# Kernel optimization log

Measured on AMD Instinct MI355X. Metric: run time of the kernel, lower is better.

The kernel has to match this reference:

```python
import jax, jax.numpy as jnp
import numpy as np

B, N, M, DN, DE, WN, WE, P = 16, 128, 1024, 512, 256, 128, 128, 512
EMB = WN + WE            # nenn embedding size per node / per edge
CLS_IN = 2 * EMB // 1    # = 2*wn + 2*we = 512
LR_OUT, CR_OUT, MR_OUT = 9, 6, 17
HID = 256


def _mk_params(key):
    ks = jax.random.split(key, 16)
    s = 0.02
    p = {
        'Wn':  jax.random.normal(ks[0], (DN, WN), jnp.float32) * s,
        'We':  jax.random.normal(ks[1], (DE, WE), jnp.float32) * s,
        'Wn2': jax.random.normal(ks[2], (DN, WN), jnp.float32) * s,
        'We2': jax.random.normal(ks[3], (DE, WE), jnp.float32) * s,
    }
    for i, h in enumerate(['scr', 'lr', 'mr']):
        out = {'scr': CR_OUT, 'lr': LR_OUT, 'mr': MR_OUT}[h]
        p[h + '_W1'] = jax.random.normal(ks[4 + 4 * i], (2 * EMB, HID), jnp.float32) * s
        p[h + '_b1'] = jnp.zeros((HID,), jnp.float32)
        p[h + '_W2'] = jax.random.normal(ks[5 + 4 * i], (HID, out), jnp.float32) * s
        p[h + '_b2'] = jnp.zeros((out,), jnp.float32)
    return p


def setup_inputs() -> dict:
    key = jax.random.key(0)
    ks = jax.random.split(key, 10)
    inp = {
        'node_features': jax.random.normal(ks[0], (B, N, DN), jnp.float32),
        'edge_features': jax.random.normal(ks[1], (B, N, N, DE), jnp.float32),
        'adj_mat': (jax.random.uniform(ks[2], (B, N, N)) < 0.1).astype(jnp.float32),
        'line_adj_mat': (jax.random.uniform(ks[3], (B, M, M)) < 0.02).astype(jnp.float32),
        'edge_index': jax.random.randint(ks[4], (B, 2, M), 0, N, jnp.int32),
        'object_pairs': jax.random.randint(ks[5], (B, P, 2), 0, N, jnp.int32),
        'num_obj': jax.random.randint(ks[6], (B,), N // 4, N + 1, jnp.int32),
        'num_edges': jax.random.randint(ks[7], (B,), M // 4, M + 1, jnp.int32),
    }
    inp.update(_mk_params(ks[8]))
    return inp


def _mlp(x, W1, b1, W2, b2):
    return jax.nn.relu(x @ W1 + b1) @ W2 + b2


def _forward(node_features, edge_features, adj_mat, line_adj_mat,
             Wn, We, Wn2, We2,
             scr_W1, scr_b1, scr_W2, scr_b2,
             lr_W1, lr_b1, lr_W2, lr_b2,
             mr_W1, mr_b1, mr_W2, mr_b2,
             edge_index, object_pairs, num_obj, num_edges):
    dt = node_features.dtype
    # ragged slicing [:num_obj] / [:num_edges] expressed as masks (padding stays 0)
    nmask = (jnp.arange(N) < num_obj[:, None]).astype(dt)      # [B,N]
    emask = (jnp.arange(M) < num_edges[:, None]).astype(dt)    # [B,M]

    X = node_features * nmask[..., None]                        # [B,N,DN]
    A = (adj_mat * nmask[:, :, None] * nmask[:, None, :]
         + jnp.eye(N, dtype=dt)[None] * nmask[:, :, None])      # A + I, masked
    h = jax.nn.relu((A @ X) @ Wn) * nmask[..., None]            # [B,N,WN] node-level emb

    src, dst = edge_index[:, 0], edge_index[:, 1]               # [B,M]
    Eg = jax.vmap(lambda e, s, d: e[s, d])(edge_features, src, dst)  # [B,M,DE]
    Eg = Eg * emask[..., None]
    L = (line_adj_mat * emask[:, :, None] * emask[:, None, :]
         + jnp.eye(M, dtype=dt)[None] * emask[:, :, None])      # line graph A + I
    g = jax.nn.relu((L @ Eg) @ We) * emask[..., None]           # [B,M,WE] edge-level emb

    # aggregate edge embeddings onto their source nodes (ragged scatter-add)
    agg = jax.vmap(lambda gb, sb: jnp.zeros((N, WE), gb.dtype).at[sb].add(gb))(g, src)
    node_emb = jnp.concatenate([h, agg * nmask[..., None]], -1)  # [B,N,EMB]

    # dense pairwise edge embeddings [B,N,N,EMB]
    Xp = X @ Wn2                                                 # [B,N,WN]
    Pm = jax.nn.relu(Xp[:, :, None, :] + Xp[:, None, :, :])      # node part [B,N,N,WN]
    Q = jax.nn.relu(edge_features @ We2)                         # edge part [B,N,N,WE]
    edge_emb = jnp.concatenate([Pm, Q], -1)

    # make_classifier_inputs: fused ragged gather instead of python double loop
    p0, p1 = object_pairs[..., 0], object_pairs[..., 1]          # [B,P]
    emb0 = jnp.take_along_axis(node_emb, p0[:, :, None], axis=1)  # [B,P,EMB]
    emb1 = jnp.take_along_axis(node_emb, p1[:, :, None], axis=1)
    eedge = jax.vmap(lambda eb, a, b: eb[a, b])(edge_emb, p0, p1)  # [B,P,EMB]
    ci = jnp.concatenate([emb0 + emb1, eedge], -1)               # aggregator='sum'

    lr = _mlp(ci, lr_W1, lr_b1, lr_W2, lr_b2)
    cr = _mlp(ci, scr_W1, scr_b1, scr_W2, scr_b2)
    mr = _mlp(ci, mr_W1, mr_b1, mr_W2, mr_b2)
    return lr, cr, mr


def reference(node_features, edge_features, adj_mat, line_adj_mat,
              edge_index, object_pairs, num_obj, num_edges,
              Wn, We, Wn2, We2,
              scr_W1, scr_b1, scr_W2, scr_b2,
              lr_W1, lr_b1, lr_W2, lr_b2,
              mr_W1, mr_b1, mr_W2, mr_b2):
    return _forward(node_features, edge_features, adj_mat, line_adj_mat,
                    Wn, We, Wn2, We2,
                    scr_W1, scr_b1, scr_W2, scr_b2,
                    lr_W1, lr_b1, lr_W2, lr_b2,
                    mr_W1, mr_b1, mr_W2, mr_b2,
                    edge_index, object_pairs, num_obj, num_edges)
```

## Files before the change

### kernel.cpp

```cpp
#include <hip/hip_runtime.h>
#include <hip/hip_bf16.h>
#include <cstdint>
#include <cstddef>

#define BB 16
#define NN 128
#define MM 1024
#define DN 512
#define DE 256
#define WN 128
#define WE 128
#define PP 512
#define HIDW 256
#define CIW 512

typedef __attribute__((ext_vector_type(8))) short s16x8;
typedef __attribute__((ext_vector_type(4))) float f32x4;

__device__ __forceinline__ float bf2f(unsigned short u) {
    unsigned int x = ((unsigned int)u) << 16;
    union { unsigned int i; float f; } c; c.i = x; return c.f;
}

__global__ __launch_bounds__(256) void k0_prep(
    const float* __restrict__ lrW1, const float* __restrict__ scrW1,
    const float* __restrict__ mrW1,
    const float* __restrict__ lrb1, const float* __restrict__ scrb1,
    const float* __restrict__ mrb1,
    __hip_bfloat16* __restrict__ W1t, float* __restrict__ b1cat)
{
    int blk = blockIdx.x;
    int t = threadIdx.x;
    if (blk < 768) {
        int h = blk >> 8, n = blk & 255;
        const float* W = (h == 0) ? lrW1 : (h == 1) ? scrW1 : mrW1;
        W1t[(size_t)blk * 512 + t]       = __float2bfloat16(W[t * 256 + n]);
        W1t[(size_t)blk * 512 + t + 256] = __float2bfloat16(W[(t + 256) * 256 + n]);
    } else {
        b1cat[t]       = lrb1[t];
        b1cat[256 + t] = scrb1[t];
        b1cat[512 + t] = mrb1[t];
    }
}

__global__ __launch_bounds__(256) void k1_node_proj(
    const float* __restrict__ nf, const float* __restrict__ Wn,
    const float* __restrict__ Wn2, const int* __restrict__ num_obj,
    float* __restrict__ Y, float* __restrict__ Xp)
{
    __shared__ float Xs[16 * 513];
    int b  = blockIdx.x >> 4;
    int i0 = ((blockIdx.x >> 1) & 7) * 16;
    int ch = blockIdx.x & 1;
    int s  = num_obj[b];
    int t  = threadIdx.x;
    for (int rr = 0; rr < 16; ++rr) {
        int i = i0 + rr;
        const float* row = nf + (size_t)(b * NN + i) * DN;
        Xs[rr * 513 + t]       = (i < s) ? row[t]       : 0.f;
        Xs[rr * 513 + t + 256] = (i < s) ? row[t + 256] : 0.f;
    }
    __syncthreads();
    int c  = ch * 64 + (t & 63);
    int rb = (t >> 6) * 4;
    float a1[4] = {0.f,0.f,0.f,0.f}, a2[4] = {0.f,0.f,0.f,0.f};
    for (int k = 0; k < DN; ++k) {
        float w1 = Wn[k * WN + c];
        float w2 = Wn2[k * WN + c];
        #pragma unroll
        for (int r = 0; r < 4; ++r) {
            float xv = Xs[(rb + r) * 513 + k];
            a1[r] += xv * w1;
            a2[r] += xv * w2;
        }
    }
    #pragma unroll
    for (int r = 0; r < 4; ++r) {
        int i = i0 + rb + r;
        Y [(b * NN + i) * WN + c] = a1[r];
        Xp[(b * NN + i) * WN + c] = a2[r];
    }
}

__global__ __launch_bounds__(256) void k2_gcn_node(
    const float* __restrict__ adj, const int* __restrict__ num_obj,
    const float* __restrict__ Y, float* __restrict__ node_emb)
{
    __shared__ float As[16 * 129];
    int b  = blockIdx.x >> 4;
    int i0 = ((blockIdx.x >> 1) & 7) * 16;
    int ch = blockIdx.x & 1;
    int s  = num_obj[b];
    int t  = threadIdx.x;
    if (t < 128) {
        for (int rr = 0; rr < 16; ++rr) {
            int i = i0 + rr;
            float v = 0.f;
            if (i < s) {
                v = adj[(size_t)(b * NN + i) * NN + t] * ((t < s) ? 1.f : 0.f);
                if (t == i) v += 1.f;
            }
            As[rr * 129 + t] = v;
        }
    }
    __syncthreads();
    int c  = ch * 64 + (t & 63);
    int rb = (t >> 6) * 4;
    float acc[4] = {0.f,0.f,0.f,0.f};
    for (int j = 0; j < NN; ++j) {
        float yv = Y[(b * NN + j) * WN + c];
        #pragma unroll
        for (int r = 0; r < 4; ++r) acc[r] += As[(rb + r) * 129 + j] * yv;
    }
    #pragma unroll
    for (int r = 0; r < 4; ++r) {
        int i = i0 + rb + r;
        node_emb[(b * NN + i) * 256 + c]       = fmaxf(acc[r], 0.f);
        node_emb[(b * NN + i) * 256 + 128 + c] = 0.f;
    }
}

__global__ __launch_bounds__(256) void k3_edge_proj(
    const float* __restrict__ ef, const float* __restrict__ We,
    const int* __restrict__ eidx, const int* __restrict__ num_edges,
    float* __restrict__ G1)
{
    __shared__ float Es[16 * 257];
    int b  = blockIdx.x >> 6;
    int m0 = (blockIdx.x & 63) * 16;
    int se = num_edges[b];
    int t  = threadIdx.x;
    for (int rr = 0; rr < 16; ++rr) {
        int m = m0 + rr;
        float v = 0.f;
        if (m < se) {
            int src = eidx[b * 2 * MM + m];
            int dst = eidx[b * 2 * MM + MM + m];
            v = ef[((size_t)(b * NN + src) * NN + dst) * DE + t];
        }
        Es[rr * 257 + t] = v;
    }
    __syncthreads();
    int c  = t & 127;
    int rb = (t >> 7) * 8;
    float acc[8];
    #pragma unroll
    for (int r = 0; r < 8; ++r) acc[r] = 0.f;
    for (int k = 0; k < DE; ++k) {
        float wv = We[k * WE + c];
        #pragma unroll
        for (int r = 0; r < 8; ++r) acc[r] += Es[(rb + r) * 257 + k] * wv;
    }
    #pragma unroll
    for (int r = 0; r < 8; ++r)
        G1[(size_t)(b * MM + m0 + rb + r) * WE + c] = acc[r];
}

__global__ __launch_bounds__(128) void k4_line_gcn(
    const float* __restrict__ la, const float* __restrict__ G1,
    const int* __restrict__ eidx, const int* __restrict__ num_edges,
    float* __restrict__ node_emb)
{
    int b = blockIdx.x >> 10;
    int m = blockIdx.x & 1023;
    int se = num_edges[b];
    if (m >= se) return;
    __shared__ int   cnt;
    __shared__ int   idxs[MM];
    __shared__ float vals[MM];
    int t = threadIdx.x;
    if (t == 0) cnt = 0;
    __syncthreads();
    const float* larow = la + ((size_t)b * MM + m) * MM;
    for (int it = 0; it < 8; ++it) {
        int j = it * 128 + t;
        float v = larow[j];
        if (v != 0.f) {
            int pos = atomicAdd(&cnt, 1);
            idxs[pos] = j;
            vals[pos] = v;
        }
    }
    __syncthreads();
    int n = cnt;
    const float* g1b = G1 + (size_t)b * MM * WE;
    float acc = g1b[m * WE + t];
    for (int p = 0; p < n; ++p)
        acc += vals[p] * g1b[idxs[p] * WE + t];
    float g = fmaxf(acc, 0.f);
    int src = eidx[b * 2 * MM + m];
    atomicAdd(&node_emb[(b * NN + src) * 256 + 128 + t], g);
}

__global__ __launch_bounds__(256) void k5a_build_ci(
    const float* __restrict__ node_emb, const float* __restrict__ Xp,
    const float* __restrict__ ef, const float* __restrict__ We2,
    const int* __restrict__ opairs, const int* __restrict__ num_obj,
    __hip_bfloat16* __restrict__ ci)
{
    __shared__ float efs[16 * 257];
    __shared__ int   pi0[16], pi1[16];
    __shared__ float nm0[16], nm1[16];
    int b     = blockIdx.x >> 5;
    int pbase = (blockIdx.x & 31) * 16;
    int t     = threadIdx.x;
    int s     = num_obj[b];
    if (t < 16) {
        int p  = pbase + t;
        int i0 = opairs[(b * PP + p) * 2];
        int i1 = opairs[(b * PP + p) * 2 + 1];
        pi0[t] = i0; pi1[t] = i1;
        nm0[t] = (i0 < s) ? 1.f : 0.f;
        nm1[t] = (i1 < s) ? 1.f : 0.f;
    }
    __syncthreads();
    for (int pp = 0; pp < 16; ++pp) {
        int i0 = pi0[pp], i1 = pi1[pp];
        int p  = pbase + pp;
        __hip_bfloat16* cirow = ci + (size_t)(b * PP + p) * CIW;
        efs[pp * 257 + t] = ef[((size_t)(b * NN + i0) * NN + i1) * DE + t];
        float m0f = (t < 128) ? 1.f : nm0[pp];
        float m1f = (t < 128) ? 1.f : nm1[pp];
        float v = node_emb[(b * NN + i0) * 256 + t] * m0f
                + node_emb[(b * NN + i1) * 256 + t] * m1f;
        cirow[t] = __float2bfloat16(v);
        if (t < 128) {
            float pm = Xp[(b * NN + i0) * WN + t] + Xp[(b * NN + i1) * WN + t];
            cirow[256 + t] = __float2bfloat16(fmaxf(pm, 0.f));
        }
    }
    __syncthreads();
    int c   = t & 127;
    int ppb = (t >> 7) * 8;
    float acc[8];
    #pragma unroll
    for (int r = 0; r < 8; ++r) acc[r] = 0.f;
    for (int k = 0; k < DE; ++k) {
        float wv = We2[k * WE + c];
        #pragma unroll
        for (int r = 0; r < 8; ++r) acc[r] += efs[(ppb + r) * 257 + k] * wv;
    }
    #pragma unroll
    for (int r = 0; r < 8; ++r) {
        int p = pbase + ppb + r;
        ci[(size_t)(b * PP + p) * CIW + 384 + c] = __float2bfloat16(fmaxf(acc[r], 0.f));
    }
}

__global__ __launch_bounds__(256) void k6_mlp1_mfma(
    const ushort* __restrict__ A,
    const ushort* __restrict__ Bt,
    const float* __restrict__ b1cat,
    __hip_bfloat16* __restrict__ H)
{
    __shared__ ushort As[128 * 32];
    __shared__ ushort Bs[128 * 32];
    int t    = threadIdx.x;
    int col0 = blockIdx.x * 128;
    int row0 = blockIdx.y * 128;
    int lane = t & 63;
    int w    = t >> 6;
    int wr   = w >> 1, wc = w & 1;
    int arow = w * 32 + (lane >> 2);
    int ak   = (lane & 3) * 8;
    int qk   = (lane >> 4) * 8;
    int fr   = lane & 15;
    f32x4 acc[4][4];
    #pragma unroll
    for (int i = 0; i < 4; ++i)
        #pragma unroll
        for (int j = 0; j < 4; ++j) acc[i][j] = (f32x4){0.f, 0.f, 0.f, 0.f};

    for (int k0 = 0; k0 < CIW; k0 += 32) {
        __syncthreads();
        *(s16x8*)&As[arow * 32 + ak] =
            *(const s16x8*)&A[(size_t)(row0 + arow) * CIW + k0 + ak];
        *(s16x8*)&As[(arow + 16) * 32 + ak] =
            *(const s16x8*)&A[(size_t)(row0 + arow + 16) * CIW + k0 + ak];
        *(s16x8*)&Bs[arow * 32 + ak] =
            *(const s16x8*)&Bt[(size_t)(col0 + arow) * CIW + k0 + ak];
        *(s16x8*)&Bs[(arow + 16) * 32 + ak] =
            *(const s16x8*)&Bt[(size_t)(col0 + arow + 16) * CIW + k0 + ak];
        __syncthreads();
        s16x8 af[4], bfv[4];
        #pragma unroll
        for (int mi = 0; mi < 4; ++mi)
            af[mi] = *(const s16x8*)&As[(wr * 64 + mi * 16 + fr) * 32 + qk];
        #pragma unroll
        for (int ni = 0; ni < 4; ++ni)
            bfv[ni] = *(const s16x8*)&Bs[(wc * 64 + ni * 16 + fr) * 32 + qk];
        #pragma unroll
        for (int mi = 0; mi < 4; ++mi)
            #pragma unroll
            for (int ni = 0; ni < 4; ++ni)
                acc[mi][ni] = __builtin_amdgcn_mfma_f32_16x16x32_bf16(
                    af[mi], bfv[ni], acc[mi][ni], 0, 0, 0);
    }
    int crow = (lane >> 4) * 4;
    #pragma unroll
    for (int mi = 0; mi < 4; ++mi) {
        #pragma unroll
        for (int ni = 0; ni < 4; ++ni) {
            int gc = col0 + wc * 64 + ni * 16 + fr;
            int gr = row0 + wr * 64 + mi * 16 + crow;
            float bias = b1cat[gc];
            #pragma unroll
            for (int rg = 0; rg < 4; ++rg) {
                float v = fmaxf(acc[mi][ni][rg] + bias, 0.f);
                H[(size_t)(gr + rg) * 768 + gc] = __float2bfloat16(v);
            }
        }
    }
}

__global__ __launch_bounds__(256) void k7_mlp2(
    const __hip_bfloat16* __restrict__ H,
    const float* __restrict__ lrW2, const float* __restrict__ lrb2,
    const float* __restrict__ scrW2, const float* __restrict__ scrb2,
    const float* __restrict__ mrW2, const float* __restrict__ mrb2,
    float* __restrict__ outp)
{
    __shared__ float w2s[32 * 257];
    int t = threadIdx.x;
    for (int o = 0; o < 32; ++o) {
        float v;
        if (o < 9)       v = lrW2[t * 9 + o];
        else if (o < 15) v = scrW2[t * 6 + (o - 9)];
        else             v = mrW2[t * 17 + (o - 15)];
        w2s[o * 257 + t] = v;
    }
    __syncthreads();
    int p = blockIdx.x * 8 + (t >> 5);
    int o = t & 31;
    int seg = (o < 9) ? 0 : ((o < 15) ? 1 : 2);
    const ushort* hr = (const ushort*)H + (size_t)p * 768 + seg * 256;
    const float* wr = &w2s[o * 257];
    float acc = (o < 9) ? lrb2[o] : ((o < 15) ? scrb2[o - 9] : mrb2[o - 15]);
    for (int k = 0; k < HIDW; k += 2) {
        ushort2 u = *(const ushort2*)&hr[k];
        acc += bf2f(u.x) * wr[k] + bf2f(u.y) * wr[k + 1];
    }
    if (o < 9)       outp[(size_t)p * 9 + o] = acc;
    else if (o < 15) outp[8192 * 9 + (size_t)p * 6 + (o - 9)] = acc;
    else             outp[8192 * 15 + (size_t)p * 17 + (o - 15)] = acc;
}

extern "C" void kernel_launch(void* const* d_in, const int* in_sizes, int n_in,
                              void* d_out, int out_size, void* d_ws, size_t ws_size,
                              hipStream_t stream) {
    const float* nf    = (const float*)d_in[0];
    const float* ef    = (const float*)d_in[1];
    const float* adj   = (const float*)d_in[2];
    const float* la    = (const float*)d_in[3];
    const int*   eidx  = (const int*)d_in[4];
    const int*   opair = (const int*)d_in[5];
    const int*   nobj  = (const int*)d_in[6];
    const int*   nedg  = (const int*)d_in[7];
    const float* Wn    = (const float*)d_in[8];
    const float* We    = (const float*)d_in[9];
    const float* Wn2   = (const float*)d_in[10];
    const float* We2   = (const float*)d_in[11];
    const float* scrW1 = (const float*)d_in[12];
    const float* scrb1 = (const float*)d_in[13];
    const float* scrW2 = (const float*)d_in[14];
    const float* scrb2 = (const float*)d_in[15];
    const float* lrW1  = (const float*)d_in[16];
    const float* lrb1  = (const float*)d_in[17];
    const float* lrW2  = (const float*)d_in[18];
    const float* lrb2  = (const float*)d_in[19];
    const float* mrW1  = (const float*)d_in[20];
    const float* mrb1  = (const float*)d_in[21];
    const float* mrW2  = (const float*)d_in[22];
    const float* mrb2  = (const float*)d_in[23];

    float* ws = (float*)d_ws;
    float* Y        = ws;
    float* Xp       = Y + 262144;
    float* node_emb = Xp + 262144;
    float* G1       = node_emb + 524288;
    __hip_bfloat16* ci  = (__hip_bfloat16*)(G1 + 2097152);
    __hip_bfloat16* hid = (__hip_bfloat16*)(G1 + 2097152 + 2097152);
    __hip_bfloat16* W1t = (__hip_bfloat16*)(G1 + 2097152 + 2097152 + 3145728);
    float* b1cat    = (float*)(W1t) + 196608;

    k0_prep     <<<769, 256, 0, stream>>>(lrW1, scrW1, mrW1, lrb1, scrb1, mrb1,
                                          W1t, b1cat);
    k1_node_proj<<<BB * 8 * 2, 256, 0, stream>>>(nf, Wn, Wn2, nobj, Y, Xp);
    k2_gcn_node <<<BB * 8 * 2, 256, 0, stream>>>(adj, nobj, Y, node_emb);
    k3_edge_proj<<<BB * (MM / 16), 256, 0, stream>>>(ef, We, eidx, nedg, G1);
    k4_line_gcn <<<BB * MM, 128, 0, stream>>>(la, G1, eidx, nedg, node_emb);
    k5a_build_ci<<<BB * (PP / 16), 256, 0, stream>>>(node_emb, Xp, ef, We2,
                                                     opair, nobj, ci);
    k6_mlp1_mfma<<<dim3(6, 64), 256, 0, stream>>>((const ushort*)ci,
                                                  (const ushort*)W1t, b1cat, hid);
    k7_mlp2     <<<8192 / 8, 256, 0, stream>>>(hid, lrW2, lrb2, scrW2, scrb2,
                                               mrW2, mrb2, (float*)d_out);
}
```

Before: 557.2 us.

## Fuse node, edge and pair projections into one bf16 MFMA gather-GEMM kernel

Replaces the three scalar FP32 projection GEMMs (node features by Wn/Wn2, gathered edge features by We, pair edge features by We2) with a single launch that routes blocks to one of three GEMMs. Each block gathers rows through per-row offsets, applies the validity mask and converts to bf16 before using 16x16x32 bf16 MFMA. The weights are transposed to bf16 in the prep kernel. This removes slow scalar FMA loops and two launches, at the cost of bf16 rounding of the projection inputs and an unpipelined single-buffered K loop.

```diff
diff --git a/kernel.cpp b/kernel.cpp
--- a/kernel.cpp
+++ b/kernel.cpp
@@ -21,13 +21,21 @@
     unsigned int x = ((unsigned int)u) << 16;
     union { unsigned int i; float f; } c; c.i = x; return c.f;
 }
+__device__ __forceinline__ short f2b(float f) {
+    __hip_bfloat16 h = __float2bfloat16(f);
+    return *reinterpret_cast<short*>(&h);
+}
 
 __global__ __launch_bounds__(256) void k0_prep(
     const float* __restrict__ lrW1, const float* __restrict__ scrW1,
     const float* __restrict__ mrW1,
     const float* __restrict__ lrb1, const float* __restrict__ scrb1,
     const float* __restrict__ mrb1,
-    __hip_bfloat16* __restrict__ W1t, float* __restrict__ b1cat)
+    const float* __restrict__ Wn, const float* __restrict__ Wn2,
+    const float* __restrict__ We, const float* __restrict__ We2,
+    __hip_bfloat16* __restrict__ W1t, __hip_bfloat16* __restrict__ WncT,
+    __hip_bfloat16* __restrict__ WeT, __hip_bfloat16* __restrict__ We2T,
+    float* __restrict__ b1cat)
 {
     int blk = blockIdx.x;
     int t = threadIdx.x;
@@ -36,49 +44,143 @@
         const float* W = (h == 0) ? lrW1 : (h == 1) ? scrW1 : mrW1;
         W1t[(size_t)blk * 512 + t]       = __float2bfloat16(W[t * 256 + n]);
         W1t[(size_t)blk * 512 + t + 256] = __float2bfloat16(W[(t + 256) * 256 + n]);
-    } else {
+    } else if (blk == 768) {
         b1cat[t]       = lrb1[t];
         b1cat[256 + t] = scrb1[t];
         b1cat[512 + t] = mrb1[t];
-    }
-}
-
-__global__ __launch_bounds__(256) void k1_node_proj(
-    const float* __restrict__ nf, const float* __restrict__ Wn,
-    const float* __restrict__ Wn2, const int* __restrict__ num_obj,
-    float* __restrict__ Y, float* __restrict__ Xp)
-{
-    __shared__ float Xs[16 * 513];
-    int b  = blockIdx.x >> 4;
-    int i0 = ((blockIdx.x >> 1) & 7) * 16;
-    int ch = blockIdx.x & 1;
-    int s  = num_obj[b];
-    int t  = threadIdx.x;
-    for (int rr = 0; rr < 16; ++rr) {
-        int i = i0 + rr;
-        const float* row = nf + (size_t)(b * NN + i) * DN;
-        Xs[rr * 513 + t]       = (i < s) ? row[t]       : 0.f;
-        Xs[rr * 513 + t + 256] = (i < s) ? row[t + 256] : 0.f;
-    }
-    __syncthreads();
-    int c  = ch * 64 + (t & 63);
-    int rb = (t >> 6) * 4;
-    float a1[4] = {0.f,0.f,0.f,0.f}, a2[4] = {0.f,0.f,0.f,0.f};
-    for (int k = 0; k < DN; ++k) {
-        float w1 = Wn[k * WN + c];
-        float w2 = Wn2[k * WN + c];
-        #pragma unroll
-        for (int r = 0; r < 4; ++r) {
-            float xv = Xs[(rb + r) * 513 + k];
-            a1[r] += xv * w1;
-            a2[r] += xv * w2;
-        }
-    }
+    } else if (blk < 897) {
+        int n = blk - 769;
+        WeT[(size_t)n * 256 + t] = __float2bfloat16(We[t * 128 + n]);
+    } else if (blk < 1153) {
+        int n = blk - 897;
+        const float* W = (n < 128) ? Wn : Wn2;
+        int c = n & 127;
+        WncT[(size_t)n * 512 + t]       = __float2bfloat16(W[t * 128 + c]);
+        WncT[(size_t)n * 512 + t + 256] = __float2bfloat16(W[(t + 256) * 128 + c]);
+    } else {
+        int n = blk - 1153;
+        We2T[(size_t)n * 256 + t] = __float2bfloat16(We2[t * 128 + n]);
+    }
+}
+
+__global__ __launch_bounds__(256) void fproj(
+    const float* __restrict__ nf, const float* __restrict__ ef,
+    const int* __restrict__ eidx, const int* __restrict__ opair,
+    const int* __restrict__ nobj, const int* __restrict__ nedg,
+    const ushort* __restrict__ WncT, const ushort* __restrict__ WeT,
+    const ushort* __restrict__ We2T,
+    float* __restrict__ Y, float* __restrict__ Xp,
+    float* __restrict__ G1, __hip_bfloat16* __restrict__ ci)
+{
+    __shared__ ushort As[128 * 32];
+    __shared__ ushort Bs[128 * 32];
+    __shared__ unsigned rowoff[128];
+    __shared__ float    rowval[128];
+
+    int blk = blockIdx.x;
+    int route, mb, nb, K;
+    const ushort* Bt;
+    if (blk < 32)       { route = 0; mb = blk >> 1;  nb = blk & 1; K = 512; Bt = WncT; }
+    else if (blk < 160) { route = 1; mb = blk - 32;  nb = 0;       K = 256; Bt = WeT;  }
+    else                { route = 2; mb = blk - 160; nb = 0;       K = 256; Bt = We2T; }
+    int row0 = mb * 128, col0 = nb * 128;
+    int t = threadIdx.x;
+
+    if (t < 128) {
+        int r = row0 + t;
+        unsigned off; float valid = 1.f;
+        if (route == 0) {
+            int b = r >> 7, i = r & 127;
+            off = (unsigned)r * DN;
+            valid = (i < nobj[b]) ? 1.f : 0.f;
+        } else if (route == 1) {
+            int b = r >> 10, m = r & 1023;
+            int src = eidx[b * 2 * MM + m];
+            int dst = eidx[b * 2 * MM + MM + m];
+            off = (unsigned)((b * NN + src) * NN + dst) * DE;
+            valid = (m < nedg[b]) ? 1.f : 0.f;
+        } else {
+            int r2 = r;
+            int b = r2 >> 9, p = r2 & 511;
+            int i0 = opair[(b * PP + p) * 2];
+            int i1 = opair[(b * PP + p) * 2 + 1];
+            off = (unsigned)((b * NN + i0) * NN + i1) * DE;
+        }
+        rowoff[t] = off; rowval[t] = valid;
+    }
+
+    const float* Asrc = (route == 0) ? nf : ef;
+    int lane = t & 63;
+    int w    = t >> 6;
+    int wr   = w >> 1, wc = w & 1;
+    int arow = w * 32 + (lane >> 2);
+    int ak   = (lane & 3) * 8;
+    int qk   = (lane >> 4) * 8;
+    int fr   = lane & 15;
+    f32x4 acc[4][4];
     #pragma unroll
-    for (int r = 0; r < 4; ++r) {
-        int i = i0 + rb + r;
-        Y [(b * NN + i) * WN + c] = a1[r];
-        Xp[(b * NN + i) * WN + c] = a2[r];
+    for (int i = 0; i < 4; ++i)
+        #pragma unroll
+        for (int j = 0; j < 4; ++j) acc[i][j] = (f32x4){0.f, 0.f, 0.f, 0.f};
+
+    for (int k0 = 0; k0 < K; k0 += 32) {
+        __syncthreads();
+        {
+            unsigned o0 = rowoff[arow] + k0 + ak;
+            unsigned o1 = rowoff[arow + 16] + k0 + ak;
+            float m0 = rowval[arow], m1 = rowval[arow + 16];
+            float4 a0 = *(const float4*)&Asrc[o0];
+            float4 a1 = *(const float4*)&Asrc[o0 + 4];
+            float4 b0 = *(const float4*)&Asrc[o1];
+            float4 b1 = *(const float4*)&Asrc[o1 + 4];
+            s16x8 pa, pb;
+            pa[0]=f2b(a0.x*m0); pa[1]=f2b(a0.y*m0); pa[2]=f2b(a0.z*m0); pa[3]=f2b(a0.w*m0);
+            pa[4]=f2b(a1.x*m0); pa[5]=f2b(a1.y*m0); pa[6]=f2b(a1.z*m0); pa[7]=f2b(a1.w*m0);
+            pb[0]=f2b(b0.x*m1); pb[1]=f2b(b0.y*m1); pb[2]=f2b(b0.z*m1); pb[3]=f2b(b0.w*m1);
+            pb[4]=f2b(b1.x*m1); pb[5]=f2b(b1.y*m1); pb[6]=f2b(b1.z*m1); pb[7]=f2b(b1.w*m1);
+            *(s16x8*)&As[arow * 32 + ak]        = pa;
+            *(s16x8*)&As[(arow + 16) * 32 + ak] = pb;
+            *(s16x8*)&Bs[arow * 32 + ak] =
+                *(const s16x8*)&Bt[(size_t)(col0 + arow) * K + k0 + ak];
+            *(s16x8*)&Bs[(arow + 16) * 32 + ak] =
+                *(const s16x8*)&Bt[(size_t)(col0 + arow + 16) * K + k0 + ak];
+        }
+        __syncthreads();
+        s16x8 af[4], bfv[4];
+        #pragma unroll
+        for (int mi = 0; mi < 4; ++mi)
+            af[mi] = *(const s16x8*)&As[(wr * 64 + mi * 16 + fr) * 32 + qk];
+        #pragma unroll
+        for (int ni = 0; ni < 4; ++ni)
+            bfv[ni] = *(const s16x8*)&Bs[(wc * 64 + ni * 16 + fr) * 32 + qk];
+        #pragma unroll
+        for (int mi = 0; mi < 4; ++mi)
+            #pragma unroll
+            for (int ni = 0; ni < 4; ++ni)
+                acc[mi][ni] = __builtin_amdgcn_mfma_f32_16x16x32_bf16(
+                    af[mi], bfv[ni], acc[mi][ni], 0, 0, 0);
+    }
+    int crow = (lane >> 4) * 4;
+    #pragma unroll
+    for (int mi = 0; mi < 4; ++mi) {
+        #pragma unroll
+        for (int ni = 0; ni < 4; ++ni) {
+            int gc = col0 + wc * 64 + ni * 16 + fr;
+            int gr = row0 + wr * 64 + mi * 16 + crow;
+            #pragma unroll
+            for (int rg = 0; rg < 4; ++rg) {
+                float v = acc[mi][ni][rg];
+                int r = gr + rg;
+                if (route == 0) {
+                    if (gc < 128) Y [(size_t)r * WN + gc]       = v;
+                    else          Xp[(size_t)r * WN + gc - 128] = v;
+                } else if (route == 1) {
+                    G1[(size_t)r * WE + gc] = v;
+                } else {
+                    ci[(size_t)r * CIW + 384 + gc] = __float2bfloat16(fmaxf(v, 0.f));
+                }
+            }
+        }
     }
 }
 
@@ -118,42 +220,6 @@
         node_emb[(b * NN + i) * 256 + c]       = fmaxf(acc[r], 0.f);
         node_emb[(b * NN + i) * 256 + 128 + c] = 0.f;
     }
-}
-
-__global__ __launch_bounds__(256) void k3_edge_proj(
-    const float* __restrict__ ef, const float* __restrict__ We,
-    const int* __restrict__ eidx, const int* __restrict__ num_edges,
-    float* __restrict__ G1)
-{
-    __shared__ float Es[16 * 257];
-    int b  = blockIdx.x >> 6;
-    int m0 = (blockIdx.x & 63) * 16;
-    int se = num_edges[b];
-    int t  = threadIdx.x;
-    for (int rr = 0; rr < 16; ++rr) {
-        int m = m0 + rr;
-        float v = 0.f;
-        if (m < se) {
-            int src = eidx[b * 2 * MM + m];
-            int dst = eidx[b * 2 * MM + MM + m];
-            v = ef[((size_t)(b * NN + src) * NN + dst) * DE + t];
-        }
-        Es[rr * 257 + t] = v;
-    }
-    __syncthreads();
-    int c  = t & 127;
-    int rb = (t >> 7) * 8;
-    float acc[8];
-    #pragma unroll
-    for (int r = 0; r < 8; ++r) acc[r] = 0.f;
-    for (int k = 0; k < DE; ++k) {
-        float wv = We[k * WE + c];
-        #pragma unroll
-        for (int r = 0; r < 8; ++r) acc[r] += Es[(rb + r) * 257 + k] * wv;
-    }
-    #pragma unroll
-    for (int r = 0; r < 8; ++r)
-        G1[(size_t)(b * MM + m0 + rb + r) * WE + c] = acc[r];
 }
 
 __global__ __launch_bounds__(128) void k4_line_gcn(
@@ -194,11 +260,9 @@
 
 __global__ __launch_bounds__(256) void k5a_build_ci(
     const float* __restrict__ node_emb, const float* __restrict__ Xp,
-    const float* __restrict__ ef, const float* __restrict__ We2,
     const int* __restrict__ opairs, const int* __restrict__ num_obj,
     __hip_bfloat16* __restrict__ ci)
 {
-    __shared__ float efs[16 * 257];
     __shared__ int   pi0[16], pi1[16];
     __shared__ float nm0[16], nm1[16];
     int b     = blockIdx.x >> 5;
@@ -218,7 +282,6 @@
         int i0 = pi0[pp], i1 = pi1[pp];
         int p  = pbase + pp;
         __hip_bfloat16* cirow = ci + (size_t)(b * PP + p) * CIW;
-        efs[pp * 257 + t] = ef[((size_t)(b * NN + i0) * NN + i1) * DE + t];
         float m0f = (t < 128) ? 1.f : nm0[pp];
         float m1f = (t < 128) ? 1.f : nm1[pp];
         float v = node_emb[(b * NN + i0) * 256 + t] * m0f
@@ -228,22 +291,6 @@
             float pm = Xp[(b * NN + i0) * WN + t] + Xp[(b * NN + i1) * WN + t];
             cirow[256 + t] = __float2bfloat16(fmaxf(pm, 0.f));
         }
-    }
-    __syncthreads();
-    int c   = t & 127;
-    int ppb = (t >> 7) * 8;
-    float acc[8];
-    #pragma unroll
-    for (int r = 0; r < 8; ++r) acc[r] = 0.f;
-    for (int k = 0; k < DE; ++k) {
-        float wv = We2[k * WE + c];
-        #pragma unroll
-        for (int r = 0; r < 8; ++r) acc[r] += efs[(ppb + r) * 257 + k] * wv;
-    }
-    #pragma unroll
-    for (int r = 0; r < 8; ++r) {
-        int p = pbase + ppb + r;
-        ci[(size_t)(b * PP + p) * CIW + 384 + c] = __float2bfloat16(fmaxf(acc[r], 0.f));
     }
 }
 
@@ -378,19 +425,24 @@
     float* Xp       = Y + 262144;
     float* node_emb = Xp + 262144;
     float* G1       = node_emb + 524288;
-    __hip_bfloat16* ci  = (__hip_bfloat16*)(G1 + 2097152);
-    __hip_bfloat16* hid = (__hip_bfloat16*)(G1 + 2097152 + 2097152);
-    __hip_bfloat16* W1t = (__hip_bfloat16*)(G1 + 2097152 + 2097152 + 3145728);
-    float* b1cat    = (float*)(W1t) + 196608;
-
-    k0_prep     <<<769, 256, 0, stream>>>(lrW1, scrW1, mrW1, lrb1, scrb1, mrb1,
-                                          W1t, b1cat);
-    k1_node_proj<<<BB * 8 * 2, 256, 0, stream>>>(nf, Wn, Wn2, nobj, Y, Xp);
+    float* base     = G1 + 2097152;
+    __hip_bfloat16* ci   = (__hip_bfloat16*)base;
+    __hip_bfloat16* hid  = (__hip_bfloat16*)(base + 2097152);
+    __hip_bfloat16* W1t  = (__hip_bfloat16*)(base + 2097152 + 3145728);
+    __hip_bfloat16* WncT = (__hip_bfloat16*)(base + 2097152 + 3145728 + 196608);
+    __hip_bfloat16* WeT  = (__hip_bfloat16*)(base + 2097152 + 3145728 + 196608 + 65536);
+    __hip_bfloat16* We2T = (__hip_bfloat16*)(base + 2097152 + 3145728 + 196608 + 65536 + 16384);
+    float* b1cat = base + 2097152 + 3145728 + 196608 + 65536 + 16384 + 16384;
+
+    k0_prep <<<1281, 256, 0, stream>>>(lrW1, scrW1, mrW1, lrb1, scrb1, mrb1,
+                                       Wn, Wn2, We, We2,
+                                       W1t, WncT, WeT, We2T, b1cat);
+    fproj   <<<224, 256, 0, stream>>>(nf, ef, eidx, opair, nobj, nedg,
+                                      (const ushort*)WncT, (const ushort*)WeT,
+                                      (const ushort*)We2T, Y, Xp, G1, ci);
     k2_gcn_node <<<BB * 8 * 2, 256, 0, stream>>>(adj, nobj, Y, node_emb);
-    k3_edge_proj<<<BB * (MM / 16), 256, 0, stream>>>(ef, We, eidx, nedg, G1);
     k4_line_gcn <<<BB * MM, 128, 0, stream>>>(la, G1, eidx, nedg, node_emb);
-    k5a_build_ci<<<BB * (PP / 16), 256, 0, stream>>>(node_emb, Xp, ef, We2,
-                                                     opair, nobj, ci);
+    k5a_build_ci<<<BB * (PP / 16), 256, 0, stream>>>(node_emb, Xp, opair, nobj, ci);
     k6_mlp1_mfma<<<dim3(6, 64), 256, 0, stream>>>((const ushort*)ci,
                                                   (const ushort*)W1t, b1cat, hid);
     k7_mlp2     <<<8192 / 8, 256, 0, stream>>>(hid, lrW2, lrb2, scrW2, scrb2,
```

New measurement: 475.0 us. 1.17x faster.
